# Kernel tuning notes

Hardware: AMD Instinct MI355X
Metric: run time of the kernel (lower is better)

## Reference

```python
import jax, jax.numpy as jnp
import numpy as np

HIDDEN = 1024
HEADS = 16
HEAD_DIM = HIDDEN // HEADS


def setup_inputs() -> dict:
    key = jax.random.key(0)
    ks = jax.random.split(key, 9)
    B, S = 2, 2048
    std = 0.02
    inp = {
        "query": jax.random.normal(ks[0], (B, S, HIDDEN), dtype=jnp.float32),
        "Wq": jax.random.normal(ks[1], (HIDDEN, HIDDEN), dtype=jnp.float32) * std,
        "bq": jnp.zeros((HIDDEN,), dtype=jnp.float32),
        "Wk": jax.random.normal(ks[2], (HIDDEN, HIDDEN), dtype=jnp.float32) * std,
        "bk": jnp.zeros((HIDDEN,), dtype=jnp.float32),
        "Wv": jax.random.normal(ks[3], (HIDDEN, HIDDEN), dtype=jnp.float32) * std,
        "bv": jnp.zeros((HIDDEN,), dtype=jnp.float32),
        "Wo": jax.random.normal(ks[4], (HIDDEN, HIDDEN), dtype=jnp.float32) * std,
        "bo": jnp.zeros((HIDDEN,), dtype=jnp.float32),
    }
    return inp


def reference(query, Wq, bq, Wk, bk, Wv, bv, Wo, bo):
    B, S, H = query.shape
    # torch nn.Linear: y = x @ W.T + b
    Q = query @ Wq.T + bq
    K = query @ Wk.T + bk  # key defaults to query (self-attention)
    V = query @ Wv.T + bv
    # [B, S, H] -> [B, heads, S, head_dim]
    def split_heads(x):
        return x.reshape(B, S, HEADS, HEAD_DIM).transpose(0, 2, 1, 3)
    Qh, Kh, Vh = split_heads(Q), split_heads(K), split_heads(V)
    scale = jnp.sqrt(jnp.asarray(HEAD_DIM, dtype=query.dtype))
    scores = jnp.einsum("bhqd,bhkd->bhqk", Qh, Kh) / scale
    attn = jax.nn.softmax(scores, axis=-1)  # dropout=0 (eval)
    context = jnp.einsum("bhqk,bhkd->bhqd", attn, Vh)
    context = context.transpose(0, 2, 1, 3).reshape(B, S, H)
    output = context @ Wo.T + bo
    return output, attn
```

## Files before the change

### kernel.cpp

```cpp
#include <hip/hip_runtime.h>
#include <hip/hip_bf16.h>
#include <cstdint>

typedef __attribute__((ext_vector_type(4))) float f32x4;
typedef __attribute__((ext_vector_type(8))) short bf16x8;

__device__ __forceinline__ unsigned short f2bf(float f){
  union { float f; unsigned int u; } v; v.f = f;
  unsigned int u = v.u;
  u += 0x7FFFu + ((u >> 16) & 1u);
  return (unsigned short)(u >> 16);
}
__device__ __forceinline__ float bf2f(unsigned short s){
  union { unsigned int u; float f; } v; v.u = ((unsigned int)s) << 16;
  return v.f;
}

__global__ __launch_bounds__(256) void cvt_bf16(const float* __restrict__ in,
                                                unsigned short* __restrict__ out,
                                                int n4){
  int i = blockIdx.x * 256 + threadIdx.x;
  if (i < n4){
    float4 v = ((const float4*)in)[i];
    ushort4 o;
    o.x = f2bf(v.x); o.y = f2bf(v.y); o.z = f2bf(v.z); o.w = f2bf(v.w);
    ((ushort4*)out)[i] = o;
  }
}

__global__ __launch_bounds__(256) void qkv_gemm(
    const unsigned short* __restrict__ A,
    const unsigned short* __restrict__ W0,
    const unsigned short* __restrict__ W1,
    const unsigned short* __restrict__ W2,
    const float* __restrict__ b0,
    const float* __restrict__ b1,
    const float* __restrict__ b2,
    unsigned short* __restrict__ Qo,
    unsigned short* __restrict__ Ko,
    unsigned short* __restrict__ Vto)
{
  __shared__ unsigned short As[2][128*64];
  __shared__ unsigned short Bs[2][128*64];

  const int K = 1024;
  const int tid = threadIdx.x;
  const int l   = tid & 63;
  const int wid = tid >> 6;
  const int g   = l >> 4;
  const int li  = l & 15;
  const int widx = blockIdx.x >> 3;
  const int m0  = blockIdx.y * 128;
  const int n0  = (blockIdx.x & 7) * 128;
  const int wm  = (wid >> 1) * 64;
  const int wn  = (wid & 1) * 64;
  const int srow = tid >> 3;
  const int sck  = tid & 7;

  const unsigned short* Bw = (widx == 0) ? W0 : ((widx == 1) ? W1 : W2);
  const float* bias        = (widx == 0) ? b0 : ((widx == 1) ? b1 : b2);

  const unsigned short* Ag = A  + (size_t)(m0 + srow) * K + sck * 8;
  const unsigned short* Bg = Bw + (size_t)(n0 + srow) * K + sck * 8;

  f32x4 acc[4][4] = {};
  bf16x8 ra[4], rb[4];
  const int NT = K >> 6;

  #pragma unroll
  for (int r = 0; r < 4; ++r){
    ra[r] = *(const bf16x8*)(Ag + (size_t)(r*32) * K);
    rb[r] = *(const bf16x8*)(Bg + (size_t)(r*32) * K);
  }
  #pragma unroll
  for (int r = 0; r < 4; ++r){
    const int row = srow + r*32;
    const int ck  = sck ^ (row & 7);
    *(bf16x8*)(&As[0][row*64 + ck*8]) = ra[r];
    *(bf16x8*)(&Bs[0][row*64 + ck*8]) = rb[r];
  }
  __syncthreads();

  int cur = 0;
  for (int kt = 0; kt < NT; ++kt){
    if (kt + 1 < NT){
      const int kof = (kt + 1) << 6;
      #pragma unroll
      for (int r = 0; r < 4; ++r){
        ra[r] = *(const bf16x8*)(Ag + (size_t)(r*32) * K + kof);
        rb[r] = *(const bf16x8*)(Bg + (size_t)(r*32) * K + kof);
      }
    }
    #pragma unroll
    for (int kk = 0; kk < 2; ++kk){
      bf16x8 af[4], bfr[4];
      #pragma unroll
      for (int f = 0; f < 4; ++f){
        const int rowa = wm + f*16 + li;
        const int cka  = (kk*4 + g) ^ (rowa & 7);
        af[f] = *(const bf16x8*)(&As[cur][rowa*64 + cka*8]);
        const int rowb = wn + f*16 + li;
        const int ckb  = (kk*4 + g) ^ (rowb & 7);
        bfr[f] = *(const bf16x8*)(&Bs[cur][rowb*64 + ckb*8]);
      }
      #pragma unroll
      for (int fm = 0; fm < 4; ++fm)
        #pragma unroll
        for (int fn = 0; fn < 4; ++fn)
          acc[fm][fn] = __builtin_amdgcn_mfma_f32_16x16x32_bf16(af[fm], bfr[fn], acc[fm][fn], 0, 0, 0);
    }
    __syncthreads();
    if (kt + 1 < NT){
      #pragma unroll
      for (int r = 0; r < 4; ++r){
        const int row = srow + r*32;
        const int ck  = sck ^ (row & 7);
        *(bf16x8*)(&As[cur^1][row*64 + ck*8]) = ra[r];
        *(bf16x8*)(&Bs[cur^1][row*64 + ck*8]) = rb[r];
      }
      __syncthreads();
    }
    cur ^= 1;
  }

  unsigned short* Oqk = (widx == 0) ? Qo : Ko;
  #pragma unroll
  for (int fn = 0; fn < 4; ++fn){
    const int col = n0 + wn + fn*16 + li;
    const float bv = bias[col];
    #pragma unroll
    for (int fm = 0; fm < 4; ++fm){
      #pragma unroll
      for (int j = 0; j < 4; ++j){
        const int row = m0 + wm + fm*16 + g*4 + j;
        const float v = acc[fm][fn][j] + bv;
        if (widx < 2){
          Oqk[(size_t)row * 1024 + col] = f2bf(v);
        } else {
          const int bb = row >> 11;
          const int s  = row & 2047;
          Vto[((size_t)(bb*1024 + col)) * 2048 + s] = f2bf(v);
        }
      }
    }
  }
}

__global__ __launch_bounds__(256) void gemm_bt(
    const unsigned short* __restrict__ A,
    const unsigned short* __restrict__ Bw,
    const float* __restrict__ bias,
    float* __restrict__ outp,
    int M, int N, int K)
{
  __shared__ unsigned short As[2][128*64];
  __shared__ unsigned short Bs[2][128*64];

  const int tid = threadIdx.x;
  const int l   = tid & 63;
  const int wid = tid >> 6;
  const int g   = l >> 4;
  const int li  = l & 15;
  const int m0  = blockIdx.y * 128;
  const int n0  = blockIdx.x * 128;
  const int wm  = (wid >> 1) * 64;
  const int wn  = (wid & 1) * 64;
  const int srow = tid >> 3;
  const int sck  = tid & 7;

  const unsigned short* Ag = A  + (size_t)(m0 + srow) * K + sck * 8;
  const unsigned short* Bg = Bw + (size_t)(n0 + srow) * K + sck * 8;

  f32x4 acc[4][4] = {};
  bf16x8 ra[4], rb[4];
  const int NT = K >> 6;

  #pragma unroll
  for (int r = 0; r < 4; ++r){
    ra[r] = *(const bf16x8*)(Ag + (size_t)(r*32) * K);
    rb[r] = *(const bf16x8*)(Bg + (size_t)(r*32) * K);
  }
  #pragma unroll
  for (int r = 0; r < 4; ++r){
    const int row = srow + r*32;
    const int ck  = sck ^ (row & 7);
    *(bf16x8*)(&As[0][row*64 + ck*8]) = ra[r];
    *(bf16x8*)(&Bs[0][row*64 + ck*8]) = rb[r];
  }
  __syncthreads();

  int cur = 0;
  for (int kt = 0; kt < NT; ++kt){
    if (kt + 1 < NT){
      const int kof = (kt + 1) << 6;
      #pragma unroll
      for (int r = 0; r < 4; ++r){
        ra[r] = *(const bf16x8*)(Ag + (size_t)(r*32) * K + kof);
        rb[r] = *(const bf16x8*)(Bg + (size_t)(r*32) * K + kof);
      }
    }
    #pragma unroll
    for (int kk = 0; kk < 2; ++kk){
      bf16x8 af[4], bfr[4];
      #pragma unroll
      for (int f = 0; f < 4; ++f){
        const int rowa = wm + f*16 + li;
        const int cka  = (kk*4 + g) ^ (rowa & 7);
        af[f] = *(const bf16x8*)(&As[cur][rowa*64 + cka*8]);
        const int rowb = wn + f*16 + li;
        const int ckb  = (kk*4 + g) ^ (rowb & 7);
        bfr[f] = *(const bf16x8*)(&Bs[cur][rowb*64 + ckb*8]);
      }
      #pragma unroll
      for (int fm = 0; fm < 4; ++fm)
        #pragma unroll
        for (int fn = 0; fn < 4; ++fn)
          acc[fm][fn] = __builtin_amdgcn_mfma_f32_16x16x32_bf16(af[fm], bfr[fn], acc[fm][fn], 0, 0, 0);
    }
    __syncthreads();
    if (kt + 1 < NT){
      #pragma unroll
      for (int r = 0; r < 4; ++r){
        const int row = srow + r*32;
        const int ck  = sck ^ (row & 7);
        *(bf16x8*)(&As[cur^1][row*64 + ck*8]) = ra[r];
        *(bf16x8*)(&Bs[cur^1][row*64 + ck*8]) = rb[r];
      }
      __syncthreads();
    }
    cur ^= 1;
  }

  #pragma unroll
  for (int fn = 0; fn < 4; ++fn){
    const int col = n0 + wn + fn*16 + li;
    const float bv = bias[col];
    #pragma unroll
    for (int fm = 0; fm < 4; ++fm){
      #pragma unroll
      for (int j = 0; j < 4; ++j){
        const int row = m0 + wm + fm*16 + g*4 + j;
        outp[(size_t)row * N + col] = acc[fm][fn][j] + bv;
      }
    }
  }
}

__global__ __launch_bounds__(512, 4) void attn_fused(
    const unsigned short* __restrict__ Qb,
    const unsigned short* __restrict__ Kb,
    const unsigned short* __restrict__ Vt,
    float* __restrict__ attn,
    unsigned short* __restrict__ ctxb)
{
  __shared__ float red[128];
  __shared__ __align__(16) unsigned short Pb[16 * 2048];
  float* ctxred = (float*)Pb;
  char*  Pbb    = (char*)Pb;

  const int tid = threadIdx.x;
  const int l   = tid & 63;
  const int w   = tid >> 6;
  const int g   = l >> 4;
  const int li  = l & 15;
  const int q0  = blockIdx.x * 16;
  const int bh  = blockIdx.y;
  const int b   = bh >> 4;
  const int h   = bh & 15;

  const size_t qrow = (size_t)(b*2048 + q0 + li) * 1024 + h*64 + g*8;
  const bf16x8 aq0 = *(const bf16x8*)(Qb + qrow);
  const bf16x8 aq1 = *(const bf16x8*)(Qb + qrow + 32);

  const unsigned short* Kbase = Kb + (size_t)(b*2048) * 1024 + h*64 + g*8;

  f32x4 s[16];
  #pragma unroll
  for (int cf = 0; cf < 16; ++cf){
    const unsigned short* kr = Kbase + (size_t)(w*256 + cf*16 + li) * 1024;
    const bf16x8 bk0 = *(const bf16x8*)(kr);
    const bf16x8 bk1 = *(const bf16x8*)(kr + 32);
    f32x4 t = {};
    t = __builtin_amdgcn_mfma_f32_16x16x32_bf16(bk0, aq0, t, 0, 0, 0);
    t = __builtin_amdgcn_mfma_f32_16x16x32_bf16(bk1, aq1, t, 0, 0, 0);
    s[cf] = t;
  }

  float ls = 0.f;
  const int swz = li << 3;
  #pragma unroll
  for (int cf = 0; cf < 16; ++cf){
    float p0 = __expf(s[cf][0] * 0.125f);
    float p1 = __expf(s[cf][1] * 0.125f);
    float p2 = __expf(s[cf][2] * 0.125f);
    float p3 = __expf(s[cf][3] * 0.125f);
    ls += p0 + p1 + p2 + p3;
    ushort4 u;
    u.x = f2bf(p0); u.y = f2bf(p1); u.z = f2bf(p2); u.w = f2bf(p3);
    const int colb = w*512 + cf*32 + g*8;
    *(ushort4*)(Pbb + li*4096 + (colb ^ swz)) = u;
  }

  ls += __shfl_xor(ls, 16);
  ls += __shfl_xor(ls, 32);
  if (l < 16) red[w*16 + l] = ls;
  __syncthreads();

  float r4[4];
  #pragma unroll
  for (int j = 0; j < 4; ++j){
    float dj = 0.f;
    #pragma unroll
    for (int ww = 0; ww < 8; ++ww) dj += red[ww*16 + g*4 + j];
    r4[j] = 1.0f / dj;
  }

  f32x4 pv[4] = {};
  const unsigned short* Vbase = Vt + (size_t)(b*1024 + h*64) * 2048 + w*256;
  #pragma unroll
  for (int kt = 0; kt < 8; ++kt){
    const int colb2 = w*512 + kt*64 + g*16;
    const ushort4 plo = *(const ushort4*)(Pbb + li*4096 + ( colb2      ^ swz));
    const ushort4 phi = *(const ushort4*)(Pbb + li*4096 + ((colb2 + 8) ^ swz));
    bf16x8 pa;
    pa[0] = plo.x; pa[1] = plo.y; pa[2] = plo.z; pa[3] = plo.w;
    pa[4] = phi.x; pa[5] = phi.y; pa[6] = phi.z; pa[7] = phi.w;
    #pragma unroll
    for (int df = 0; df < 4; ++df){
      const bf16x8 vb = *(const bf16x8*)(Vbase + (size_t)(df*16 + li) * 2048 + kt*32 + g*8);
      pv[df] = __builtin_amdgcn_mfma_f32_16x16x32_bf16(pa, vb, pv[df], 0, 0, 0);
    }
  }

  {
    #pragma unroll
    for (int rr = 0; rr < 2; ++rr){
      const int r = 2*w + rr;
      float dj = 0.f;
      #pragma unroll
      for (int ww = 0; ww < 8; ++ww) dj += red[ww*16 + r];
      const float rv = 1.0f / dj;
      const int key = r << 3;
      float* arow = attn + ((size_t)bh * 2048 + q0 + r) * 2048;
      #pragma unroll
      for (int c0 = 0; c0 < 8; ++c0){
        const int cb = c0*512 + l*8;
        const ushort4 u = *(const ushort4*)(Pbb + r*4096 + (cb ^ key));
        f32x4 o;
        o[0] = bf2f(u.x) * rv; o[1] = bf2f(u.y) * rv;
        o[2] = bf2f(u.z) * rv; o[3] = bf2f(u.w) * rv;
        __builtin_nontemporal_store(o, (f32x4*)(arow + c0*256 + l*4));
      }
    }
  }

  __syncthreads();
  #pragma unroll
  for (int df = 0; df < 4; ++df){
    #pragma unroll
    for (int j = 0; j < 4; ++j)
      ctxred[w*1024 + (g*4 + j)*64 + df*16 + li] = pv[df][j] * r4[j];
  }
  __syncthreads();
  {
    const int idx = tid * 2;
    const int r = idx >> 6;
    const int d = idx & 63;
    float v0 = 0.f, v1 = 0.f;
    #pragma unroll
    for (int ww = 0; ww < 8; ++ww){
      v0 += ctxred[ww*1024 + r*64 + d];
      v1 += ctxred[ww*1024 + r*64 + d + 1];
    }
    const unsigned int packed = (unsigned int)f2bf(v0) | ((unsigned int)f2bf(v1) << 16);
    *(unsigned int*)(ctxb + (size_t)(b*2048 + q0 + r) * 1024 + h*64 + d) = packed;
  }
}

extern "C" void kernel_launch(void* const* d_in, const int* in_sizes, int n_in,
                              void* d_out, int out_size, void* d_ws, size_t ws_size,
                              hipStream_t stream)
{
  const float* X  = (const float*)d_in[0];
  const float* Wq = (const float*)d_in[1];
  const float* bq = (const float*)d_in[2];
  const float* Wk = (const float*)d_in[3];
  const float* bk = (const float*)d_in[4];
  const float* Wv = (const float*)d_in[5];
  const float* bv = (const float*)d_in[6];
  const float* Wo = (const float*)d_in[7];
  const float* bo = (const float*)d_in[8];

  char* ws = (char*)d_ws;
  unsigned short* Xb  = (unsigned short*)(ws);
  unsigned short* Qb  = (unsigned short*)(ws + (size_t)( 8u<<20));
  unsigned short* Kbf = (unsigned short*)(ws + (size_t)(16u<<20));
  unsigned short* Vt  = (unsigned short*)(ws + (size_t)(24u<<20));
  unsigned short* Cb  = (unsigned short*)(ws + (size_t)(32u<<20));
  unsigned short* Wqb = (unsigned short*)(ws + (size_t)(40u<<20));
  unsigned short* Wkb = (unsigned short*)(ws + (size_t)(42u<<20));
  unsigned short* Wvb = (unsigned short*)(ws + (size_t)(44u<<20));
  unsigned short* Wob = (unsigned short*)(ws + (size_t)(46u<<20));

  float* out  = (float*)d_out;
  float* attn = out + (size_t)4194304;

  cvt_bf16<<<4096, 256, 0, stream>>>(X,  Xb,  1048576);
  cvt_bf16<<<1024, 256, 0, stream>>>(Wq, Wqb, 262144);
  cvt_bf16<<<1024, 256, 0, stream>>>(Wk, Wkb, 262144);
  cvt_bf16<<<1024, 256, 0, stream>>>(Wv, Wvb, 262144);
  cvt_bf16<<<1024, 256, 0, stream>>>(Wo, Wob, 262144);

  dim3 qkvgrid(24, 32);
  qkv_gemm<<<qkvgrid, 256, 0, stream>>>(Xb, Wqb, Wkb, Wvb, bq, bk, bv, Qb, Kbf, Vt);

  dim3 agrid(128, 32);
  attn_fused<<<agrid, 512, 0, stream>>>(Qb, Kbf, Vt, attn, Cb);

  dim3 ggrid(8, 32);
  gemm_bt<<<ggrid, 256, 0, stream>>>(Cb, Wob, bo, out, 4096, 1024, 1024);
}
```

Baseline: 346.7 us.

## Recompute QK^T in second pass instead of staging full probability tile in LDS

The attention kernel now computes scores twice. The first pass only accumulates softmax denominators. The second pass recomputes QK^T per 32-key chunk, normalizes the probabilities, writes the fp32 attn directly from registers, and stages only a small per-wave bf16 tile in LDS to feed the PV MFMAs. This cuts the 64KB LDS probability buffer, which could raise occupancy, and removes the LDS readback for the attn store. The cost is doubled QK MFMA work and K reloads, plus attn stores that are less coalesced (16B per lane, rows strided).

New measurement: 466.8 us. +34.7%, slower.

```diff
diff --git a/kernel.cpp b/kernel.cpp
--- a/kernel.cpp
+++ b/kernel.cpp
@@ -4,16 +4,14 @@
 
 typedef __attribute__((ext_vector_type(4))) float f32x4;
 typedef __attribute__((ext_vector_type(8))) short bf16x8;
+typedef __attribute__((ext_vector_type(2))) unsigned int u32x2;
+typedef __attribute__((ext_vector_type(4))) unsigned int u32x4;
 
 __device__ __forceinline__ unsigned short f2bf(float f){
   union { float f; unsigned int u; } v; v.f = f;
   unsigned int u = v.u;
   u += 0x7FFFu + ((u >> 16) & 1u);
   return (unsigned short)(u >> 16);
-}
-__device__ __forceinline__ float bf2f(unsigned short s){
-  union { unsigned int u; float f; } v; v.u = ((unsigned int)s) << 16;
-  return v.f;
 }
 
 __global__ __launch_bounds__(256) void cvt_bf16(const float* __restrict__ in,
@@ -254,9 +252,8 @@
     unsigned short* __restrict__ ctxb)
 {
   __shared__ float red[128];
-  __shared__ __align__(16) unsigned short Pb[16 * 2048];
-  float* ctxred = (float*)Pb;
-  char*  Pbb    = (char*)Pb;
+  __shared__ __align__(16) unsigned int stag[8192];
+  float* ctxred = (float*)stag;
 
   const int tid = threadIdx.x;
   const int l   = tid & 63;
@@ -274,8 +271,8 @@
 
   const unsigned short* Kbase = Kb + (size_t)(b*2048) * 1024 + h*64 + g*8;
 
-  f32x4 s[16];
-  #pragma unroll
+  float ls = 0.f;
+  #pragma unroll 4
   for (int cf = 0; cf < 16; ++cf){
     const unsigned short* kr = Kbase + (size_t)(w*256 + cf*16 + li) * 1024;
     const bf16x8 bk0 = *(const bf16x8*)(kr);
@@ -283,75 +280,72 @@
     f32x4 t = {};
     t = __builtin_amdgcn_mfma_f32_16x16x32_bf16(bk0, aq0, t, 0, 0, 0);
     t = __builtin_amdgcn_mfma_f32_16x16x32_bf16(bk1, aq1, t, 0, 0, 0);
-    s[cf] = t;
-  }
-
-  float ls = 0.f;
-  const int swz = li << 3;
-  #pragma unroll
-  for (int cf = 0; cf < 16; ++cf){
-    float p0 = __expf(s[cf][0] * 0.125f);
-    float p1 = __expf(s[cf][1] * 0.125f);
-    float p2 = __expf(s[cf][2] * 0.125f);
-    float p3 = __expf(s[cf][3] * 0.125f);
-    ls += p0 + p1 + p2 + p3;
-    ushort4 u;
-    u.x = f2bf(p0); u.y = f2bf(p1); u.z = f2bf(p2); u.w = f2bf(p3);
-    const int colb = w*512 + cf*32 + g*8;
-    *(ushort4*)(Pbb + li*4096 + (colb ^ swz)) = u;
-  }
-
+    ls += __expf(t[0] * 0.125f) + __expf(t[1] * 0.125f)
+        + __expf(t[2] * 0.125f) + __expf(t[3] * 0.125f);
+  }
   ls += __shfl_xor(ls, 16);
   ls += __shfl_xor(ls, 32);
   if (l < 16) red[w*16 + l] = ls;
   __syncthreads();
 
-  float r4[4];
-  #pragma unroll
-  for (int j = 0; j < 4; ++j){
-    float dj = 0.f;
-    #pragma unroll
-    for (int ww = 0; ww < 8; ++ww) dj += red[ww*16 + g*4 + j];
-    r4[j] = 1.0f / dj;
-  }
-
+  float dsum = 0.f;
+  #pragma unroll
+  for (int ww = 0; ww < 8; ++ww) dsum += red[ww*16 + li];
+  const float rv = 1.0f / dsum;
+
+  unsigned int* ms = stag + w*320;
   f32x4 pv[4] = {};
   const unsigned short* Vbase = Vt + (size_t)(b*1024 + h*64) * 2048 + w*256;
-  #pragma unroll
-  for (int kt = 0; kt < 8; ++kt){
-    const int colb2 = w*512 + kt*64 + g*16;
-    const ushort4 plo = *(const ushort4*)(Pbb + li*4096 + ( colb2      ^ swz));
-    const ushort4 phi = *(const ushort4*)(Pbb + li*4096 + ((colb2 + 8) ^ swz));
-    bf16x8 pa;
-    pa[0] = plo.x; pa[1] = plo.y; pa[2] = plo.z; pa[3] = plo.w;
-    pa[4] = phi.x; pa[5] = phi.y; pa[6] = phi.z; pa[7] = phi.w;
-    #pragma unroll
-    for (int df = 0; df < 4; ++df){
-      const bf16x8 vb = *(const bf16x8*)(Vbase + (size_t)(df*16 + li) * 2048 + kt*32 + g*8);
-      pv[df] = __builtin_amdgcn_mfma_f32_16x16x32_bf16(pa, vb, pv[df], 0, 0, 0);
-    }
-  }
-
-  {
-    #pragma unroll
-    for (int rr = 0; rr < 2; ++rr){
-      const int r = 2*w + rr;
-      float dj = 0.f;
-      #pragma unroll
-      for (int ww = 0; ww < 8; ++ww) dj += red[ww*16 + r];
-      const float rv = 1.0f / dj;
-      const int key = r << 3;
-      float* arow = attn + ((size_t)bh * 2048 + q0 + r) * 2048;
-      #pragma unroll
-      for (int c0 = 0; c0 < 8; ++c0){
-        const int cb = c0*512 + l*8;
-        const ushort4 u = *(const ushort4*)(Pbb + r*4096 + (cb ^ key));
-        f32x4 o;
-        o[0] = bf2f(u.x) * rv; o[1] = bf2f(u.y) * rv;
-        o[2] = bf2f(u.z) * rv; o[3] = bf2f(u.w) * rv;
-        __builtin_nontemporal_store(o, (f32x4*)(arow + c0*256 + l*4));
-      }
-    }
+  float* arow = attn + ((size_t)bh * 2048 + q0 + li) * 2048 + w*256;
+
+  #pragma unroll
+  for (int ch = 0; ch < 8; ++ch){
+    const unsigned short* kr0 = Kbase + (size_t)(w*256 + ch*32 +      li) * 1024;
+    const unsigned short* kr1 = Kbase + (size_t)(w*256 + ch*32 + 16 + li) * 1024;
+    const bf16x8 a00 = *(const bf16x8*)(kr0);
+    const bf16x8 a01 = *(const bf16x8*)(kr0 + 32);
+    const bf16x8 a10 = *(const bf16x8*)(kr1);
+    const bf16x8 a11 = *(const bf16x8*)(kr1 + 32);
+    f32x4 s0 = {}, s1 = {};
+    s0 = __builtin_amdgcn_mfma_f32_16x16x32_bf16(a00, aq0, s0, 0, 0, 0);
+    s0 = __builtin_amdgcn_mfma_f32_16x16x32_bf16(a01, aq1, s0, 0, 0, 0);
+    s1 = __builtin_amdgcn_mfma_f32_16x16x32_bf16(a10, aq0, s1, 0, 0, 0);
+    s1 = __builtin_amdgcn_mfma_f32_16x16x32_bf16(a11, aq1, s1, 0, 0, 0);
+
+    f32x4 p0, p1;
+    #pragma unroll
+    for (int j = 0; j < 4; ++j){
+      p0[j] = __expf(s0[j] * 0.125f) * rv;
+      p1[j] = __expf(s1[j] * 0.125f) * rv;
+    }
+
+    *(f32x4*)(arow + ch*32 +      g*4) = p0;
+    *(f32x4*)(arow + ch*32 + 16 + g*4) = p1;
+
+    const unsigned int u0 = (unsigned int)f2bf(p0[0]) | ((unsigned int)f2bf(p0[1]) << 16);
+    const unsigned int u1 = (unsigned int)f2bf(p0[2]) | ((unsigned int)f2bf(p0[3]) << 16);
+    const unsigned int u2 = (unsigned int)f2bf(p1[0]) | ((unsigned int)f2bf(p1[1]) << 16);
+    const unsigned int u3 = (unsigned int)f2bf(p1[2]) | ((unsigned int)f2bf(p1[3]) << 16);
+    u32x2 w0; w0[0] = u0; w0[1] = u1;
+    u32x2 w1; w1[0] = u2; w1[1] = u3;
+    *(u32x2*)(ms + li*20 +     g*2) = w0;
+    *(u32x2*)(ms + li*20 + 8 + g*2) = w1;
+
+    const bf16x8 vb0 = *(const bf16x8*)(Vbase + (size_t)(     li) * 2048 + ch*32 + g*8);
+    const bf16x8 vb1 = *(const bf16x8*)(Vbase + (size_t)(16 + li) * 2048 + ch*32 + g*8);
+    const bf16x8 vb2 = *(const bf16x8*)(Vbase + (size_t)(32 + li) * 2048 + ch*32 + g*8);
+    const bf16x8 vb3 = *(const bf16x8*)(Vbase + (size_t)(48 + li) * 2048 + ch*32 + g*8);
+
+    asm volatile("s_waitcnt lgkmcnt(0)" ::: "memory");
+    __builtin_amdgcn_sched_barrier(0);
+
+    const u32x4 pk = *(const u32x4*)(ms + li*20 + g*4);
+    const bf16x8 pa = __builtin_bit_cast(bf16x8, pk);
+
+    pv[0] = __builtin_amdgcn_mfma_f32_16x16x32_bf16(pa, vb0, pv[0], 0, 0, 0);
+    pv[1] = __builtin_amdgcn_mfma_f32_16x16x32_bf16(pa, vb1, pv[1], 0, 0, 0);
+    pv[2] = __builtin_amdgcn_mfma_f32_16x16x32_bf16(pa, vb2, pv[2], 0, 0, 0);
+    pv[3] = __builtin_amdgcn_mfma_f32_16x16x32_bf16(pa, vb3, pv[3], 0, 0, 0);
   }
 
   __syncthreads();
@@ -359,7 +353,7 @@
   for (int df = 0; df < 4; ++df){
     #pragma unroll
     for (int j = 0; j < 4; ++j)
-      ctxred[w*1024 + (g*4 + j)*64 + df*16 + li] = pv[df][j] * r4[j];
+      ctxred[w*1024 + (g*4 + j)*64 + df*16 + li] = pv[df][j];
   }
   __syncthreads();
   {
```
